# Kernel tuning notes

Hardware: AMD Instinct MI355X
Metric: run time of the kernel (lower is better)

The kernel has to match this reference:

```python
import jax, jax.numpy as jnp
import numpy as np

# Longformer-base-4096 config (layers reduced 12->4 for CPU tractability)
B_, S_, DM, H_, DH, L_, FF, V = 1, 4096, 768, 12, 64, 4, 3072, 50265
BLOCK = 256  # one-sided window; total attention window = 512


def layer_norm(x, g, b, eps=1e-5):
    m = jnp.mean(x, axis=-1, keepdims=True)
    v = jnp.mean(jnp.square(x - m), axis=-1, keepdims=True)
    return (x - m) * jax.lax.rsqrt(v + eps) * g + b


def sliding_attention(q, k, v, key_mask):
    """Banded local attention: each query attends keys within +/- BLOCK positions.
    q,k,v: (B,H,S,Dh); key_mask: (B,S) 1 for valid tokens."""
    B, H, S, D = q.shape
    nb = S // BLOCK
    qb = q.reshape(B, H, nb, BLOCK, D)
    kp = jnp.pad(k, ((0, 0), (0, 0), (BLOCK, BLOCK), (0, 0)))
    vp = jnp.pad(v, ((0, 0), (0, 0), (BLOCK, BLOCK), (0, 0)))
    # each query block n sees key blocks n-1, n, n+1  -> window of 3*BLOCK keys
    idx = jnp.arange(nb)[:, None] * BLOCK + jnp.arange(3 * BLOCK)[None, :]  # (nb, 3B)
    kw = kp[:, :, idx]  # (B,H,nb,3B,D)
    vw = vp[:, :, idx]
    scores = jnp.einsum('bhnqd,bhnkd->bhnqk', qb, kw) / np.float32(np.sqrt(D))
    # relative position of key w.r.t. query inside the 3-block window
    rel = jnp.arange(3 * BLOCK)[None, :] - BLOCK - jnp.arange(BLOCK)[:, None]  # (BLOCK,3B)
    band = (jnp.abs(rel) <= BLOCK)[None, None, None]  # (1,1,1,BLOCK,3B)
    mp = jnp.pad(key_mask.astype(bool), ((0, 0), (BLOCK, BLOCK)))
    mw = mp[:, idx][:, None, :, None, :]  # (B,1,nb,1,3B)
    scores = jnp.where(band & mw, scores, -1e9)
    probs = jax.nn.softmax(scores, axis=-1)
    out = jnp.einsum('bhnqk,bhnkd->bhnqd', probs, vw)
    return out.reshape(B, H, S, D)


def encode(ids, mask, word_emb, pos_emb, emb_g, emb_b, layers):
    B, S = ids.shape
    x = word_emb[ids] + pos_emb[None, :S]
    x = layer_norm(x, emb_g, emb_b)

    def step(x, p):
        wq, bq, wk, bk, wv, bv, wo, bo, g1, b1, w1, c1, w2, c2, g2, b2 = p
        heads = lambda y: y.reshape(B, S, H_, DH).transpose(0, 2, 1, 3)
        q = heads(x @ wq + bq)
        k = heads(x @ wk + bk)
        vv = heads(x @ wv + bv)
        a = sliding_attention(q, k, vv, mask)
        a = a.transpose(0, 2, 1, 3).reshape(B, S, DM) @ wo + bo
        x2 = layer_norm(x + a, g1, b1)  # post-LN (RoBERTa/Longformer)
        h = jax.nn.gelu(x2 @ w1 + c1)
        x3 = layer_norm(x2 + h @ w2 + c2, g2, b2)
        return x3, None

    x, _ = jax.lax.scan(jax.checkpoint(step), x, layers)
    return x


def setup_inputs() -> dict:
    key = jax.random.key(0)
    ks = jax.random.split(key, 16)
    s = 0.02
    d = {
        'input_ids1': jax.random.randint(ks[0], (B_, S_), 0, V),
        'input_ids2': jax.random.randint(ks[1], (B_, S_), 0, V),
        'attention_mask1': jnp.ones((B_, S_), dtype=jnp.int32),
        'attention_mask2': jnp.ones((B_, S_), dtype=jnp.int32),
        'word_emb': jax.random.normal(ks[2], (V, DM)) * s,
        'pos_emb': jax.random.normal(ks[3], (S_, DM)) * s,
        'emb_g': jnp.ones((DM,)), 'emb_b': jnp.zeros((DM,)),
        'wq': jax.random.normal(ks[4], (L_, DM, DM)) * s, 'bq': jnp.zeros((L_, DM)),
        'wk': jax.random.normal(ks[5], (L_, DM, DM)) * s, 'bk': jnp.zeros((L_, DM)),
        'wv': jax.random.normal(ks[6], (L_, DM, DM)) * s, 'bv': jnp.zeros((L_, DM)),
        'wo': jax.random.normal(ks[7], (L_, DM, DM)) * s, 'bo': jnp.zeros((L_, DM)),
        'ln1_g': jnp.ones((L_, DM)), 'ln1_b': jnp.zeros((L_, DM)),
        'w_ff1': jax.random.normal(ks[8], (L_, DM, FF)) * s, 'b_ff1': jnp.zeros((L_, FF)),
        'w_ff2': jax.random.normal(ks[9], (L_, FF, DM)) * s, 'b_ff2': jnp.zeros((L_, DM)),
        'ln2_g': jnp.ones((L_, DM)), 'ln2_b': jnp.zeros((L_, DM)),
        'dense_w': jax.random.normal(ks[10], (DM, 1)) * s, 'dense_b': jnp.zeros((1,)),
    }
    return d


def reference(input_ids1, input_ids2, attention_mask1, attention_mask2,
              word_emb, pos_emb, emb_g, emb_b,
              wq, bq, wk, bk, wv, bv, wo, bo,
              ln1_g, ln1_b, w_ff1, b_ff1, w_ff2, b_ff2, ln2_g, ln2_b,
              dense_w, dense_b):
    layers = (wq, bq, wk, bk, wv, bv, wo, bo, ln1_g, ln1_b,
              w_ff1, b_ff1, w_ff2, b_ff2, ln2_g, ln2_b)
    o1 = encode(input_ids1, attention_mask1, word_emb, pos_emb, emb_g, emb_b, layers)
    o2 = encode(input_ids2, attention_mask2, word_emb, pos_emb, emb_g, emb_b, layers)
    diff = o1.mean(1, keepdims=True) - o2.mean(1, keepdims=True)  # (B,1,DM)
    return jax.nn.sigmoid(diff @ dense_w + dense_b)  # (B,1,1)
```

## Files before the change

### kernel.cpp

```cpp
#include <hip/hip_runtime.h>

typedef __bf16 bf16_t;
typedef bf16_t bf16x8 __attribute__((ext_vector_type(8)));
typedef float f32x4 __attribute__((ext_vector_type(4)));
typedef unsigned short u16x4 __attribute__((ext_vector_type(4)));
typedef unsigned short u16x8 __attribute__((ext_vector_type(8)));
typedef float f32x4v __attribute__((ext_vector_type(4)));

#define NL 4

__device__ __forceinline__ float bf2f(unsigned short u){
  unsigned int x = ((unsigned int)u) << 16;
  return __builtin_bit_cast(float, x);
}
__device__ __forceinline__ unsigned short f2bf(float f){
  unsigned int u = __builtin_bit_cast(unsigned int, f);
  u += 0x7FFFu + ((u >> 16) & 1u);
  return (unsigned short)(u >> 16);
}
__device__ __forceinline__ void gload16(const void* g, void* l){
  __builtin_amdgcn_global_load_lds((const __attribute__((address_space(1))) unsigned int*)g,
                                   (__attribute__((address_space(3))) unsigned int*)l, 16, 0, 0);
}

__global__ __launch_bounds__(256) void transpose_cvt16(const float* __restrict__ wq,
                                                       const float* __restrict__ wk,
                                                       const float* __restrict__ wv,
                                                       const float* __restrict__ wo,
                                                       unsigned short* __restrict__ wqkvT,
                                                       unsigned short* __restrict__ woT){
  __shared__ unsigned short tile[64][72];
  const int zi = blockIdx.z;
  const size_t W = (size_t)768 * 768;
  const float* src = (zi < 4 ? wq : zi < 8 ? wk : zi < 12 ? wv : wo) + (size_t)(zi & 3) * W;
  unsigned short* dst = (zi < 12 ? wqkvT + (size_t)zi * W : woT + (size_t)(zi - 12) * W);
  int tc0 = blockIdx.x * 64, tr0 = blockIdx.y * 64;
  int t = threadIdx.x;
  int r = t >> 2, cs = (t & 3) * 16;
  const float* s = src + (size_t)(tr0 + r) * 768 + tc0 + cs;
  #pragma unroll
  for (int j = 0; j < 16; j += 4){
    f32x4v v = *(const f32x4v*)(s + j);
    #pragma unroll
    for (int q = 0; q < 4; q++) tile[r][cs + j + q] = f2bf(v[q]);
  }
  __syncthreads();
  int n = t >> 2;
  unsigned short* d = dst + (size_t)(tc0 + n) * 768 + tr0 + cs;
  u16x8 o0, o1;
  #pragma unroll
  for (int j = 0; j < 8; j++){ o0[j] = tile[cs + j][n]; o1[j] = tile[cs + 8 + j][n]; }
  *(u16x8*)d       = o0;
  *(u16x8*)(d + 8) = o1;
}

__global__ __launch_bounds__(256) void transpose_cvt(const float* __restrict__ src,
                                                     unsigned short* __restrict__ dst,
                                                     int R, int C){
  __shared__ unsigned short tile[64][72];
  size_t boff = (size_t)blockIdx.z * (size_t)R * (size_t)C;
  int tc0 = blockIdx.x * 64, tr0 = blockIdx.y * 64;
  int t = threadIdx.x;
  int r = t >> 2, cs = (t & 3) * 16;
  const float* s = src + boff + (size_t)(tr0 + r) * C + tc0 + cs;
  #pragma unroll
  for (int j = 0; j < 16; j += 4){
    f32x4v v = *(const f32x4v*)(s + j);
    #pragma unroll
    for (int q = 0; q < 4; q++) tile[r][cs + j + q] = f2bf(v[q]);
  }
  __syncthreads();
  int n = t >> 2;
  unsigned short* d = dst + boff + (size_t)(tc0 + n) * R + tr0 + cs;
  u16x8 o0, o1;
  #pragma unroll
  for (int j = 0; j < 8; j++){ o0[j] = tile[cs + j][n]; o1[j] = tile[cs + 8 + j][n]; }
  *(u16x8*)d       = o0;
  *(u16x8*)(d + 8) = o1;
}

template<int ACT, int STORE_MODE>
__device__ __forceinline__ void gemm_core(unsigned short* lds,
                                          const unsigned short* __restrict__ A,
                                          const unsigned short* __restrict__ BT,
                                          const float* __restrict__ bias,
                                          unsigned short* __restrict__ C,
                                          int m0, int n0, int N, int K){
  const int t = threadIdx.x;
  const int lane = t & 63;
  const int l15 = lane & 15, l4 = lane >> 4;
  const int w = t >> 6, wm = w >> 1, wn = w & 1;
  f32x4 acc[4][4] = {};
  const int rr = t >> 3;
  const int c8 = ((t & 7) ^ (rr & 7)) * 8;
  const unsigned short* Abase = A  + (size_t)(m0 + rr) * K + c8;
  const unsigned short* Bbase = BT + (size_t)(n0 + rr) * K + c8;

  auto STAGE = [&](int k0, int buf){
    unsigned short* As_ = lds + buf * 16384;
    unsigned short* Bs_ = As_ + 8192;
    #pragma unroll
    for (int it = 0; it < 4; it++){
      gload16(Abase + (size_t)(it * 32) * K + k0, As_ + (it * 256 + t) * 8);
      gload16(Bbase + (size_t)(it * 32) * K + k0, Bs_ + (it * 256 + t) * 8);
    }
  };
  auto COMPUTE = [&](int buf){
    const unsigned short* Ab = lds + buf * 16384;
    const unsigned short* Bb = Ab + 8192;
    #pragma unroll
    for (int kk = 0; kk < 2; kk++){
      bf16x8 af[4], bfr[4];
      const int cs = kk * 4;
      #pragma unroll
      for (int i = 0; i < 4; i++){
        const int ra = wm * 64 + i * 16 + l15;
        const int rb = wn * 64 + i * 16 + l15;
        const int so = ((cs + l4) ^ (l15 & 7)) * 8;
        af[i]  = *(const bf16x8*)(Ab + ra * 64 + so);
        bfr[i] = *(const bf16x8*)(Bb + rb * 64 + so);
      }
      #pragma unroll
      for (int j = 0; j < 4; j++)
        #pragma unroll
        for (int i = 0; i < 4; i++)
          acc[j][i] = __builtin_amdgcn_mfma_f32_16x16x32_bf16(bfr[j], af[i], acc[j][i], 0, 0, 0);
    }
  };

  const int S = K >> 6;
  STAGE(0, 0); STAGE(64, 1);
  int cur = 0;
  for (int k = 0; k < S - 2; k++){
    asm volatile("s_waitcnt vmcnt(8)" ::: "memory");
    __builtin_amdgcn_s_barrier();
    __builtin_amdgcn_sched_barrier(0);
    __builtin_amdgcn_s_setprio(1);
    COMPUTE(cur);
    __builtin_amdgcn_s_setprio(0);
    __builtin_amdgcn_sched_barrier(0);
    __builtin_amdgcn_s_barrier();
    STAGE((k + 2) << 6, cur);
    cur ^= 1;
  }
  asm volatile("s_waitcnt vmcnt(8)" ::: "memory");
  __builtin_amdgcn_s_barrier();
  __builtin_amdgcn_sched_barrier(0);
  __builtin_amdgcn_s_setprio(1);
  COMPUTE(cur);
  __builtin_amdgcn_s_setprio(0);
  cur ^= 1;
  asm volatile("s_waitcnt vmcnt(0)" ::: "memory");
  __builtin_amdgcn_s_barrier();
  __builtin_amdgcn_sched_barrier(0);
  __builtin_amdgcn_s_setprio(1);
  COMPUTE(cur);
  __builtin_amdgcn_s_setprio(0);

  const int mB = m0 + wm * 64;
  const int nB = n0 + wn * 64;
  if (STORE_MODE == 0){
    #pragma unroll
    for (int i = 0; i < 4; i++){
      unsigned short* crow = C + (size_t)(mB + i * 16 + l15) * N + nB;
      #pragma unroll
      for (int j = 0; j < 4; j++){
        const int nn = j * 16 + l4 * 4;
        f32x4v bb = *(const f32x4v*)(bias + nB + nn);
        u16x4 pk;
        #pragma unroll
        for (int r = 0; r < 4; r++){
          float v = acc[j][i][r] + bb[r];
          if (ACT == 1){
            float e = __expf(-1.5957691216057308f * (v + 0.044715f * v * v * v));
            v = __fdividef(v, 1.0f + e);
          }
          pk[r] = f2bf(v);
        }
        *(u16x4*)(crow + nn) = pk;
      }
    }
  } else {
    #pragma unroll
    for (int i = 0; i < 4; i++){
      const int m = mB + i * 16 + l15;
      unsigned short* vbase = C + (size_t)(m >> 12) * 768 * 4096 + (m & 4095);
      #pragma unroll
      for (int j = 0; j < 4; j++){
        const int nn = nB + j * 16 + l4 * 4;
        f32x4v bb = *(const f32x4v*)(bias + nn);
        #pragma unroll
        for (int r = 0; r < 4; r++)
          vbase[(size_t)(nn + r) * 4096] = f2bf(acc[j][i][r] + bb[r]);
      }
    }
  }
}

template<int ACT>
__global__ __launch_bounds__(256) void gemm_bt(const unsigned short* __restrict__ A,
                                               const unsigned short* __restrict__ BT,
                                               const float* __restrict__ bias,
                                               unsigned short* __restrict__ C, int N, int K){
  __shared__ unsigned short lds[32768];
  const int b = blockIdx.x;
  const int s = b >> 3;
  const int m = (b & 7) * 8 + (s & 7);
  const int n = s >> 3;
  gemm_core<ACT, 0>(lds, A, BT, bias, C, m * 128, n * 128, N, K);
}

__global__ __launch_bounds__(256) void qkv_gemm(const unsigned short* __restrict__ A,
                                                const unsigned short* __restrict__ wT,
                                                int l,
                                                const float* __restrict__ bq,
                                                const float* __restrict__ bk,
                                                const float* __restrict__ bv,
                                                unsigned short* __restrict__ q,
                                                unsigned short* __restrict__ k,
                                                unsigned short* __restrict__ vt){
  __shared__ unsigned short lds[32768];
  const int b = blockIdx.x;
  const int s = b >> 3;
  const int m0 = ((b & 7) * 8 + (s & 7)) * 128;
  const int grp = s >> 3;
  const int sel = grp / 6, col = grp % 6;
  const unsigned short* BT = wT + ((size_t)sel * NL + l) * (size_t)(768 * 768);
  if (sel == 2)      gemm_core<0, 2>(lds, A, BT, bv, vt, m0, col * 128, 768, 768);
  else               gemm_core<0, 0>(lds, A, BT, sel == 0 ? bq : bk, sel == 0 ? q : k,
                                     m0, col * 128, 768, 768);
}

__global__ __launch_bounds__(256, 4) void attn_kernel(const unsigned short* __restrict__ Q,
                                                      const unsigned short* __restrict__ Km,
                                                      const unsigned short* __restrict__ VT,
                                                      const int* __restrict__ mask1,
                                                      const int* __restrict__ mask2,
                                                      unsigned short* __restrict__ O){
  const int qt = blockIdx.x, h = blockIdx.y, seq = blockIdx.z;
  const int t = threadIdx.x, lane = t & 63, w = t >> 6;
  const int l15 = lane & 15, l4 = lane >> 4;
  __shared__ unsigned short Kc[64 * 64];
  __shared__ unsigned short VTc[64 * 64];
  __shared__ unsigned short Ps[4][16 * 64];
  const unsigned short* Qp  = Q  + (size_t)seq * 4096 * 768;
  const unsigned short* Kp  = Km + (size_t)seq * 4096 * 768;
  const unsigned short* VTp = VT + (size_t)seq * 768 * 4096;
  const int* mask = seq ? mask2 : mask1;
  unsigned short* Op = O + (size_t)seq * 4096 * 768;

  const int q0 = qt * 64 + w * 16;
  const int qg = q0 + l15;
  const int swz = (l15 & 7) * 8;

  bf16x8 qf[2];
  #pragma unroll
  for (int ks = 0; ks < 2; ks++)
    qf[ks] = *(const bf16x8*)(Qp + (size_t)qg * 768 + h * 64 + ks * 32 + l4 * 8);

  f32x4 oacc[4] = {};
  float rm = -1e30f, rl = 0.0f;

  const int kstart = qt * 64 >= 256 ? qt * 64 - 256 : 0;
  const int kend0  = qt * 64 + 320;
  const int kend   = kend0 > 4096 ? 4096 : kend0;
  unsigned short* psw = &Ps[w][0];

  const int rr = t >> 3;
  const int c8 = (((t & 7) ^ (rr & 7)) * 8);

  for (int kb = kstart; kb < kend; kb += 64){
    gload16(Kp  + (size_t)(kb + rr) * 768 + h * 64 + c8,       Kc + t * 8);
    gload16(Kp  + (size_t)(kb + 32 + rr) * 768 + h * 64 + c8,  Kc + 2048 + t * 8);
    gload16(VTp + (size_t)(h * 64 + rr) * 4096 + kb + c8,      VTc + t * 8);
    gload16(VTp + (size_t)(h * 64 + 32 + rr) * 4096 + kb + c8, VTc + 2048 + t * 8);
    __syncthreads();
    if (kb + 63 >= q0 - 256 && kb <= q0 + 271){
      f32x4 sT[4];
      #pragma unroll
      for (int mt = 0; mt < 4; mt++){
        const unsigned short* kr = Kc + (mt * 16 + l15) * 64;
        bf16x8 kf0 = *(const bf16x8*)(kr + ((l4 * 8) ^ swz));
        bf16x8 kf1 = *(const bf16x8*)(kr + ((32 + l4 * 8) ^ swz));
        f32x4 z = {};
        z      = __builtin_amdgcn_mfma_f32_16x16x32_bf16(kf0, qf[0], z, 0, 0, 0);
        sT[mt] = __builtin_amdgcn_mfma_f32_16x16x32_bf16(kf1, qf[1], z, 0, 0, 0);
      }
      float smax = -1e30f;
      #pragma unroll
      for (int mt = 0; mt < 4; mt++){
        int4 mv = *(const int4*)(mask + kb + mt * 16 + l4 * 4);
        #pragma unroll
        for (int r = 0; r < 4; r++){
          int kgl = kb + mt * 16 + l4 * 4 + r;
          int d = kgl - qg;
          int mvv = (r == 0) ? mv.x : (r == 1) ? mv.y : (r == 2) ? mv.z : mv.w;
          bool ok = (mvv != 0) && (d <= 256) && (d >= -256);
          float v = sT[mt][r] * 0.125f;
          sT[mt][r] = ok ? v : -1e30f;
          smax = fmaxf(smax, sT[mt][r]);
        }
      }
      smax = fmaxf(smax, __shfl_xor(smax, 16, 64));
      smax = fmaxf(smax, __shfl_xor(smax, 32, 64));
      float nm = fmaxf(rm, smax);
      float sc = __expf(rm - nm);
      rm = nm;
      float psum = 0.0f;
      #pragma unroll
      for (int mt = 0; mt < 4; mt++){
        u16x4 pk;
        #pragma unroll
        for (int r = 0; r < 4; r++){
          float p = (sT[mt][r] > -1e29f) ? __expf(sT[mt][r] - nm) : 0.0f;
          psum += p;
          pk[r] = f2bf(p);
        }
        *(u16x4*)(psw + l15 * 64 + ((mt * 16 + l4 * 4) ^ swz)) = pk;
      }
      psum += __shfl_xor(psum, 16, 64);
      psum += __shfl_xor(psum, 32, 64);
      rl = rl * sc + psum;
      float scq[4];
      #pragma unroll
      for (int r = 0; r < 4; r++) scq[r] = __shfl(sc, l4 * 4 + r, 64);
      #pragma unroll
      for (int g = 0; g < 4; g++)
        #pragma unroll
        for (int r = 0; r < 4; r++) oacc[g][r] *= scq[r];
      asm volatile("s_waitcnt lgkmcnt(0)" ::: "memory");
      __builtin_amdgcn_sched_barrier(0);
      bf16x8 pa0 = *(const bf16x8*)(psw + l15 * 64 + ((l4 * 8) ^ swz));
      bf16x8 pa1 = *(const bf16x8*)(psw + l15 * 64 + ((32 + l4 * 8) ^ swz));
      #pragma unroll
      for (int g = 0; g < 4; g++){
        const unsigned short* vr = VTc + (g * 16 + l15) * 64;
        bf16x8 vb0 = *(const bf16x8*)(vr + ((l4 * 8) ^ swz));
        bf16x8 vb1 = *(const bf16x8*)(vr + ((32 + l4 * 8) ^ swz));
        oacc[g] = __builtin_amdgcn_mfma_f32_16x16x32_bf16(pa0, vb0, oacc[g], 0, 0, 0);
        oacc[g] = __builtin_amdgcn_mfma_f32_16x16x32_bf16(pa1, vb1, oacc[g], 0, 0, 0);
      }
    }
    __syncthreads();
  }
  float rlq[4];
  #pragma unroll
  for (int r = 0; r < 4; r++) rlq[r] = __shfl(rl, l4 * 4 + r, 64);
  #pragma unroll
  for (int g = 0; g < 4; g++)
    #pragma unroll
    for (int r = 0; r < 4; r++){
      float v = oacc[g][r] / rlq[r];
      Op[(size_t)(q0 + l4 * 4 + r) * 768 + h * 64 + g * 16 + l15] = f2bf(v);
    }
}

__global__ __launch_bounds__(192) void embed_ln(const int* __restrict__ ids1,
                                                const int* __restrict__ ids2,
                                                const float* __restrict__ we,
                                                const float* __restrict__ pe,
                                                const float* __restrict__ g,
                                                const float* __restrict__ b,
                                                unsigned short* __restrict__ out){
  const int row = blockIdx.x;
  const int seq = row >> 12, s = row & 4095;
  const int t = threadIdx.x;
  const int id = (seq ? ids2 : ids1)[s];
  f32x4v wvv = *(const f32x4v*)(we + (size_t)id * 768 + t * 4);
  f32x4v pv  = *(const f32x4v*)(pe + (size_t)s * 768 + t * 4);
  float v[4];
  #pragma unroll
  for (int j = 0; j < 4; j++) v[j] = wvv[j] + pv[j];
  float sum = 0, ss = 0;
  #pragma unroll
  for (int j = 0; j < 4; j++){ sum += v[j]; ss += v[j] * v[j]; }
  for (int off = 1; off < 64; off <<= 1){ sum += __shfl_xor(sum, off, 64); ss += __shfl_xor(ss, off, 64); }
  __shared__ float red[2][3];
  int wid = t >> 6;
  if ((t & 63) == 0){ red[0][wid] = sum; red[1][wid] = ss; }
  __syncthreads();
  sum = red[0][0] + red[0][1] + red[0][2];
  ss  = red[1][0] + red[1][1] + red[1][2];
  float mean = sum * (1.0f / 768.0f);
  float var  = ss * (1.0f / 768.0f) - mean * mean;
  float rstd = rsqrtf(var + 1e-5f);
  f32x4v gv = *(const f32x4v*)(g + t * 4);
  f32x4v bv = *(const f32x4v*)(b + t * 4);
  u16x4 o;
  #pragma unroll
  for (int j = 0; j < 4; j++) o[j] = f2bf((v[j] - mean) * rstd * gv[j] + bv[j]);
  *(u16x4*)(out + (size_t)row * 768 + t * 4) = o;
}

__global__ __launch_bounds__(192) void add_ln(const unsigned short* __restrict__ A,
                                              const unsigned short* __restrict__ Bp,
                                              const float* __restrict__ g,
                                              const float* __restrict__ b,
                                              unsigned short* __restrict__ out){
  const int row = blockIdx.x;
  const int t = threadIdx.x;
  u16x4 a4 = *(const u16x4*)(A  + (size_t)row * 768 + t * 4);
  u16x4 b4 = *(const u16x4*)(Bp + (size_t)row * 768 + t * 4);
  float v[4];
  #pragma unroll
  for (int j = 0; j < 4; j++) v[j] = bf2f(a4[j]) + bf2f(b4[j]);
  float sum = 0, ss = 0;
  #pragma unroll
  for (int j = 0; j < 4; j++){ sum += v[j]; ss += v[j] * v[j]; }
  for (int off = 1; off < 64; off <<= 1){ sum += __shfl_xor(sum, off, 64); ss += __shfl_xor(ss, off, 64); }
  __shared__ float red[2][3];
  int wid = t >> 6;
  if ((t & 63) == 0){ red[0][wid] = sum; red[1][wid] = ss; }
  __syncthreads();
  sum = red[0][0] + red[0][1] + red[0][2];
  ss  = red[1][0] + red[1][1] + red[1][2];
  float mean = sum * (1.0f / 768.0f);
  float var  = ss * (1.0f / 768.0f) - mean * mean;
  float rstd = rsqrtf(var + 1e-5f);
  f32x4v gv = *(const f32x4v*)(g + t * 4);
  f32x4v bv = *(const f32x4v*)(b + t * 4);
  u16x4 o;
  #pragma unroll
  for (int j = 0; j < 4; j++) o[j] = f2bf((v[j] - mean) * rstd * gv[j] + bv[j]);
  *(u16x4*)(out + (size_t)row * 768 + t * 4) = o;
}

__global__ __launch_bounds__(256) void colmean(const unsigned short* __restrict__ X,
                                               float* __restrict__ mean){
  const int t = threadIdx.x;
  const int seq = blockIdx.y;
  const int r0 = blockIdx.x * 64;
  const unsigned short* base = X + ((size_t)seq * 4096 + r0) * 768;
  float a0 = 0, a1 = 0, a2 = 0;
  for (int r = 0; r < 64; r++){
    const unsigned short* p = base + (size_t)r * 768;
    a0 += bf2f(p[t]);
    a1 += bf2f(p[t + 256]);
    a2 += bf2f(p[t + 512]);
  }
  atomicAdd(&mean[seq * 768 + t], a0);
  atomicAdd(&mean[seq * 768 + t + 256], a1);
  atomicAdd(&mean[seq * 768 + t + 512], a2);
}

__global__ __launch_bounds__(256) void final_k(const float* __restrict__ means,
                                               const float* __restrict__ dw,
                                               const float* __restrict__ db,
                                               float* __restrict__ out){
  const int t = threadIdx.x;
  float part = 0;
  for (int c = t; c < 768; c += 256)
    part += (means[c] - means[768 + c]) * (1.0f / 4096.0f) * dw[c];
  for (int off = 1; off < 64; off <<= 1) part += __shfl_xor(part, off, 64);
  __shared__ float red[4];
  if ((t & 63) == 0) red[t >> 6] = part;
  __syncthreads();
  if (t == 0){
    float r = red[0] + red[1] + red[2] + red[3] + db[0];
    out[0] = 1.0f / (1.0f + expf(-r));
  }
}

__global__ void sentinel_k(float* out){ out[0] = -1.0f; }

extern "C" void kernel_launch(void* const* d_in, const int* in_sizes, int n_in,
                              void* d_out, int out_size, void* d_ws, size_t ws_size,
                              hipStream_t stream){
  (void)in_sizes; (void)n_in; (void)out_size;
  const int* ids1  = (const int*)d_in[0];
  const int* ids2  = (const int*)d_in[1];
  const int* mask1 = (const int*)d_in[2];
  const int* mask2 = (const int*)d_in[3];
  const float* we = (const float*)d_in[4];
  const float* pe = (const float*)d_in[5];
  const float* eg = (const float*)d_in[6];
  const float* eb = (const float*)d_in[7];
  const float* wq = (const float*)d_in[8];
  const float* bq = (const float*)d_in[9];
  const float* wk = (const float*)d_in[10];
  const float* bk = (const float*)d_in[11];
  const float* wv = (const float*)d_in[12];
  const float* bv = (const float*)d_in[13];
  const float* wo = (const float*)d_in[14];
  const float* bo = (const float*)d_in[15];
  const float* g1 = (const float*)d_in[16];
  const float* b1 = (const float*)d_in[17];
  const float* w1 = (const float*)d_in[18];
  const float* c1 = (const float*)d_in[19];
  const float* w2 = (const float*)d_in[20];
  const float* c2 = (const float*)d_in[21];
  const float* g2 = (const float*)d_in[22];
  const float* b2 = (const float*)d_in[23];
  const float* dw = (const float*)d_in[24];
  const float* db = (const float*)d_in[25];
  float* outp = (float*)d_out;

  char* ws = (char*)d_ws;
  size_t off = 0;
  auto alloc = [&](size_t bytes) -> char* {
    char* p = ws + off;
    off += (bytes + 255) & ~(size_t)255;
    return p;
  };
  const size_t W768 = (size_t)768 * 768;
  const size_t WFF  = (size_t)768 * 3072;
  unsigned short* wqkvT = (unsigned short*)alloc(3 * NL * W768 * 2);
  unsigned short* woT   = (unsigned short*)alloc(NL * W768 * 2);
  unsigned short* w1T   = (unsigned short*)alloc(NL * WFF * 2);
  unsigned short* w2T   = (unsigned short*)alloc(NL * WFF * 2);
  unsigned short* xb    = (unsigned short*)alloc((size_t)8192 * 768 * 2);
  unsigned short* qb_   = (unsigned short*)alloc((size_t)8192 * 768 * 2);
  unsigned short* kb_   = (unsigned short*)alloc((size_t)8192 * 768 * 2);
  unsigned short* vb_   = (unsigned short*)alloc((size_t)8192 * 768 * 2);
  unsigned short* hb    = (unsigned short*)alloc((size_t)8192 * 3072 * 2);
  unsigned short* vt    = (unsigned short*)alloc((size_t)2 * 768 * 4096 * 2);
  float* means          = (float*)alloc(2 * 768 * 4);
  if (off > ws_size){ sentinel_k<<<1, 1, 0, stream>>>(outp); return; }

  transpose_cvt16<<<dim3(12, 12, 16), 256, 0, stream>>>(wq, wk, wv, wo, wqkvT, woT);
  transpose_cvt<<<dim3(48, 12, NL), 256, 0, stream>>>(w1, w1T, 768, 3072);
  transpose_cvt<<<dim3(12, 48, NL), 256, 0, stream>>>(w2, w2T, 3072, 768);

  embed_ln<<<8192, 192, 0, stream>>>(ids1, ids2, we, pe, eg, eb, xb);

  for (int l = 0; l < NL; l++){
    qkv_gemm<<<1152, 256, 0, stream>>>(xb, wqkvT, l, bq + l * 768, bk + l * 768, bv + l * 768,
                                       qb_, kb_, vt);
    attn_kernel<<<dim3(64, 12, 2), 256, 0, stream>>>(qb_, kb_, vt, mask1, mask2, vb_);
    gemm_bt<0><<<384, 256, 0, stream>>>(vb_, woT + (size_t)l * W768, bo + l * 768, qb_, 768, 768);
    add_ln<<<8192, 192, 0, stream>>>(xb, qb_, g1 + l * 768, b1 + l * 768, kb_);
    gemm_bt<1><<<1536, 256, 0, stream>>>(kb_, w1T + (size_t)l * WFF, c1 + l * 3072, hb, 3072, 768);
    gemm_bt<0><<<384, 256, 0, stream>>>(hb, w2T + (size_t)l * WFF, c2 + l * 768, vb_, 768, 3072);
    add_ln<<<8192, 192, 0, stream>>>(kb_, vb_, g2 + l * 768, b2 + l * 768, xb);
  }

  hipMemsetAsync(means, 0, 2 * 768 * 4, stream);
  colmean<<<dim3(64, 2), 256, 0, stream>>>(xb, means);
  final_k<<<1, 256, 0, stream>>>(means, dw, db, outp);
}
```

Measured before the change: 1.000 ms.

## Load LDS fragments before barrier and overlap next-stage global loads with MFMAs

Restructures the GEMM main loop so each iteration first reads all fragments from LDS into registers, then passes a barrier. It then issues the global->LDS prefetch for stage k+2 into the same buffer before running the MFMAs, so the loads overlap the matrix math instead of following it. The epilogue special cases are folded into the loop with conditionals. The cost is more live registers for the doubled fragment arrays, which may hurt occupancy.

Result: faster. 980.6 us (-2.0%).

```diff
diff --git a/kernel.cpp b/kernel.cpp
--- a/kernel.cpp
+++ b/kernel.cpp
@@ -105,57 +105,53 @@
       gload16(Bbase + (size_t)(it * 32) * K + k0, Bs_ + (it * 256 + t) * 8);
     }
   };
-  auto COMPUTE = [&](int buf){
+
+  bf16x8 af[2][4], bfr[2][4];
+  auto LOADFRAGS = [&](int buf){
     const unsigned short* Ab = lds + buf * 16384;
     const unsigned short* Bb = Ab + 8192;
     #pragma unroll
     for (int kk = 0; kk < 2; kk++){
-      bf16x8 af[4], bfr[4];
-      const int cs = kk * 4;
       #pragma unroll
       for (int i = 0; i < 4; i++){
-        const int ra = wm * 64 + i * 16 + l15;
-        const int rb = wn * 64 + i * 16 + l15;
-        const int so = ((cs + l4) ^ (l15 & 7)) * 8;
-        af[i]  = *(const bf16x8*)(Ab + ra * 64 + so);
-        bfr[i] = *(const bf16x8*)(Bb + rb * 64 + so);
-      }
+        const int so = ((kk * 4 + l4) ^ (l15 & 7)) * 8;
+        af[kk][i]  = *(const bf16x8*)(Ab + (wm * 64 + i * 16 + l15) * 64 + so);
+        bfr[kk][i] = *(const bf16x8*)(Bb + (wn * 64 + i * 16 + l15) * 64 + so);
+      }
+    }
+  };
+  auto MFMAS = [&](){
+    #pragma unroll
+    for (int kk = 0; kk < 2; kk++)
       #pragma unroll
       for (int j = 0; j < 4; j++)
         #pragma unroll
         for (int i = 0; i < 4; i++)
-          acc[j][i] = __builtin_amdgcn_mfma_f32_16x16x32_bf16(bfr[j], af[i], acc[j][i], 0, 0, 0);
-    }
+          acc[j][i] = __builtin_amdgcn_mfma_f32_16x16x32_bf16(bfr[kk][j], af[kk][i], acc[j][i], 0, 0, 0);
   };
 
   const int S = K >> 6;
   STAGE(0, 0); STAGE(64, 1);
+  asm volatile("s_waitcnt vmcnt(8)" ::: "memory");
+  __builtin_amdgcn_s_barrier();
   int cur = 0;
-  for (int k = 0; k < S - 2; k++){
-    asm volatile("s_waitcnt vmcnt(8)" ::: "memory");
+  for (int k = 0; k < S; k++){
+    LOADFRAGS(cur);
+    asm volatile("s_waitcnt lgkmcnt(0)" ::: "memory");
+    __builtin_amdgcn_sched_barrier(0);
     __builtin_amdgcn_s_barrier();
-    __builtin_amdgcn_sched_barrier(0);
+    if (k + 2 < S) STAGE((k + 2) << 6, cur);
     __builtin_amdgcn_s_setprio(1);
-    COMPUTE(cur);
+    MFMAS();
     __builtin_amdgcn_s_setprio(0);
     __builtin_amdgcn_sched_barrier(0);
-    __builtin_amdgcn_s_barrier();
-    STAGE((k + 2) << 6, cur);
+    if (k + 1 < S){
+      if (k + 2 < S) asm volatile("s_waitcnt vmcnt(8)" ::: "memory");
+      else           asm volatile("s_waitcnt vmcnt(0)" ::: "memory");
+      __builtin_amdgcn_s_barrier();
+    }
     cur ^= 1;
   }
-  asm volatile("s_waitcnt vmcnt(8)" ::: "memory");
-  __builtin_amdgcn_s_barrier();
-  __builtin_amdgcn_sched_barrier(0);
-  __builtin_amdgcn_s_setprio(1);
-  COMPUTE(cur);
-  __builtin_amdgcn_s_setprio(0);
-  cur ^= 1;
-  asm volatile("s_waitcnt vmcnt(0)" ::: "memory");
-  __builtin_amdgcn_s_barrier();
-  __builtin_amdgcn_sched_barrier(0);
-  __builtin_amdgcn_s_setprio(1);
-  COMPUTE(cur);
-  __builtin_amdgcn_s_setprio(0);
 
   const int mB = m0 + wm * 64;
   const int nB = n0 + wn * 64;
```
